# Optimization experiments

Measured on AMD Instinct MI355X. Metric: run time of the kernel, lower is better.

Reference implementation:

```python
import jax, jax.numpy as jnp
import numpy as np

B, N, C = 8, 4096, 1024
H = 16
D = C // H  # head_dim = 64
SCALE = D ** -0.5


def setup_inputs() -> dict:
    key = jax.random.key(0)
    ks = jax.random.split(key, 5)
    s = 0.02
    return {
        "x": jax.random.normal(ks[0], (B, N, C), dtype=jnp.float32),
        "Wq": jax.random.normal(ks[1], (C, C), dtype=jnp.float32) * s,
        "Wk": jax.random.normal(ks[2], (C, C), dtype=jnp.float32) * s,
        "Wv": jax.random.normal(ks[3], (C, C), dtype=jnp.float32) * s,
        "Wp": jax.random.normal(ks[4], (C, C), dtype=jnp.float32) * s,
        "bp": jnp.zeros((C,), dtype=jnp.float32),
    }


def reference(x, Wq, Wk, Wv, Wp, bp):
    b, n, c = x.shape
    # nn.Linear: y = x @ W^T (no bias for q/k/v)
    def split_heads(y):
        # (B,N,C) -> (B,N,H,D) -> permute(0,2,3,1) -> (B,H,D,N)
        return jnp.transpose(y.reshape(b, n, H, D), (0, 2, 3, 1))

    q = split_heads(x @ Wq.T)  # (B,H,D,N)
    k = split_heads(x @ Wk.T)  # (B,H,D,N)
    v = split_heads(x @ Wv.T)  # (B,H,D,N)

    # attn over head_dim (faithful to source layout): (B,H,D,D)
    attn = jnp.einsum('bhdn,bhen->bhde', q, k) * SCALE
    attn = jax.nn.softmax(attn, axis=-1)
    # (B,H,D,D) @ (B,H,D,N) -> (B,H,D,N); transpose(1,2) -> (B,D,H,N); reshape (B,N,C)
    out = jnp.einsum('bhde,bhen->bhdn', attn, v)
    out = jnp.transpose(out, (0, 2, 1, 3)).reshape(b, n, c)
    return out @ Wp.T + bp
```

## Files before the change

### kernel.cpp

```cpp
#include <hip/hip_runtime.h>


typedef __attribute__((ext_vector_type(4))) float f32x4;
typedef __attribute__((ext_vector_type(8))) _Float16 f16x8;
typedef __attribute__((ext_vector_type(4))) unsigned short u16x4;
typedef __attribute__((ext_vector_type(8))) unsigned short u16x8;

__device__ __forceinline__ unsigned short f2h(float f) {
  union { _Float16 h; unsigned short u; } v;
  v.h = (_Float16)f;
  return v.u;
}

__global__ void cvt_f32_f16(const float* __restrict__ in, unsigned short* __restrict__ out, int n) {
  int i = (blockIdx.x * blockDim.x + threadIdx.x) * 4;
  if (i >= n) return;
  float4 v = *(const float4*)(in + i);
  u16x4 o;
  o.x = f2h(v.x); o.y = f2h(v.y); o.z = f2h(v.z); o.w = f2h(v.w);
  *(u16x4*)(out + i) = o;
}

__global__ void cvt4_f32_f16(const float* __restrict__ s0, const float* __restrict__ s1,
                             const float* __restrict__ s2, const float* __restrict__ s3,
                             unsigned short* __restrict__ d0, unsigned short* __restrict__ d1,
                             unsigned short* __restrict__ d2, unsigned short* __restrict__ d3) {
  const float* src; unsigned short* dst;
  switch (blockIdx.y) {
    case 0: src = s0; dst = d0; break;
    case 1: src = s1; dst = d1; break;
    case 2: src = s2; dst = d2; break;
    default: src = s3; dst = d3; break;
  }
  int i = (blockIdx.x * blockDim.x + threadIdx.x) * 4;
  float4 v = *(const float4*)(src + i);
  u16x4 o;
  o.x = f2h(v.x); o.y = f2h(v.y); o.z = f2h(v.z); o.w = f2h(v.w);
  *(u16x4*)(dst + i) = o;
}

#define LDS_LD 68
enum { EPI_QKV = 0, EPI_F32_BIAS = 2 };

template <int EPI>
__global__ __launch_bounds__(256, 2) void gemm_bt(const unsigned short* __restrict__ A,
                                                  const unsigned short* __restrict__ Bt,
                                                  void* __restrict__ Cv,
                                                  const float* __restrict__ bias,
                                                  const int M, const int N, const int K) {
  __shared__ unsigned short lds[4 * 64 * LDS_LD];
  const int tid = threadIdx.x;
  const int wave = tid >> 6, lane = tid & 63;
  const int quad = lane >> 4, l15 = lane & 15;
  const int m0 = blockIdx.y * 128, n0 = blockIdx.x * 128;
  const int mb = (wave & 1) * 64, nb = (wave >> 1) * 64;

  const int sr = lane >> 2;
  const int sc = (lane & 3) ^ ((sr >> 1) & 3);

  const int swz = quad ^ ((l15 >> 1) & 3);
  int a_off[4], b_off[4];
#pragma unroll
  for (int t = 0; t < 4; t++) {
    a_off[t] = ((mb >> 4) + t) * 512 + (l15 * 4 + swz) * 8;
    b_off[t] = 4096 + ((nb >> 4) + t) * 512 + (l15 * 4 + swz) * 8;
  }

  const unsigned short* Ag = A + (size_t)(m0 + sr) * K + sc * 8;
  const unsigned short* Bg = Bt + (size_t)(n0 + sr) * K + sc * 8;

  f32x4 acc[4][4];
#pragma unroll
  for (int i = 0; i < 4; i++)
#pragma unroll
    for (int j = 0; j < 4; j++) acc[i][j] = f32x4{0.f, 0.f, 0.f, 0.f};

  for (int k0 = 0; k0 < K; k0 += 32) {
    __syncthreads();
#pragma unroll
    for (int rd = 0; rd < 2; rd++) {
      const int ch = rd * 4 + wave;
      __builtin_amdgcn_global_load_lds(
          (const __attribute__((address_space(1))) void*)(Ag + (size_t)ch * 16 * K + k0),
          (__attribute__((address_space(3))) void*)&lds[ch * 512], 16, 0, 0);
      __builtin_amdgcn_global_load_lds(
          (const __attribute__((address_space(1))) void*)(Bg + (size_t)ch * 16 * K + k0),
          (__attribute__((address_space(3))) void*)&lds[4096 + ch * 512], 16, 0, 0);
    }
    __syncthreads();

    f16x8 af[4], bf[4];
#pragma unroll
    for (int t = 0; t < 4; t++) {
      af[t] = *(const f16x8*)&lds[a_off[t]];
      bf[t] = *(const f16x8*)&lds[b_off[t]];
    }
#pragma unroll
    for (int mi = 0; mi < 4; mi++)
#pragma unroll
      for (int ni = 0; ni < 4; ni++)
        acc[mi][ni] = __builtin_amdgcn_mfma_f32_16x16x32_f16(af[mi], bf[ni], acc[mi][ni], 0, 0, 0);
  }

  __syncthreads();

  if (EPI == EPI_F32_BIAS) {
    float* C = (float*)Cv;
#pragma unroll
    for (int ni = 0; ni < 4; ni++) {
      const int col = n0 + nb + ni * 16 + l15;
      const float bv = bias[col];
#pragma unroll
      for (int mi = 0; mi < 4; mi++)
#pragma unroll
        for (int rr = 0; rr < 4; rr++) {
          const int row = m0 + mb + mi * 16 + quad * 4 + rr;
          C[(size_t)row * N + col] = acc[mi][ni][rr] + bv;
        }
    }
  } else {
    unsigned short* C = (unsigned short*)Cv;
    const bool isT = (n0 < 2048);
    unsigned short* w = &lds[wave * 64 * LDS_LD];
#pragma unroll
    for (int mi = 0; mi < 4; mi++)
#pragma unroll
      for (int ni = 0; ni < 4; ni++)
#pragma unroll
        for (int rr = 0; rr < 4; rr++) {
          const int rl = mi * 16 + quad * 4 + rr;
          const int cl = ni * 16 + l15;
          if (isT)
            w[cl * LDS_LD + rl] = f2h(acc[mi][ni][rr]);
          else
            w[rl * LDS_LD + cl] = f2h(acc[mi][ni][rr]);
        }
#pragma unroll
    for (int p = 0; p < 8; p++) {
      const int a = p * 8 + (lane >> 3);
      const int b8 = (lane & 7) * 8;
      u16x4 lo = *(const u16x4*)&w[a * LDS_LD + b8];
      u16x4 hi = *(const u16x4*)&w[a * LDS_LD + b8 + 4];
      size_t gi;
      if (isT)
        gi = (size_t)(n0 + nb + a) * M + (m0 + mb + b8);
      else
        gi = (size_t)2048 * 32768 + (size_t)(m0 + mb + a) * 1024 + (n0 - 2048 + nb + b8);
      *(u16x4*)&C[gi] = lo;
      *(u16x4*)&C[gi + 4] = hi;
    }
  }
}

__global__ __launch_bounds__(256) void attn_logits(const unsigned short* __restrict__ qkt,
                                                   float* __restrict__ pbuf) {
  const int h = blockIdx.x, b = blockIdx.y, s = blockIdx.z;
  const int tid = threadIdx.x;
  const int wave = tid >> 6, lane = tid & 63;
  const int quad = lane >> 4, l15 = lane & 15;

  f32x4 acc[4];
#pragma unroll
  for (int t = 0; t < 4; t++) acc[t] = f32x4{0.f, 0.f, 0.f, 0.f};

  const unsigned short* qp =
      qkt + (size_t)(h * 64 + wave * 16 + l15) * 32768 + b * 4096 + s * 256 + quad * 8;
  const unsigned short* kp[4];
#pragma unroll
  for (int et = 0; et < 4; et++)
    kp[et] = qkt + (size_t)(1024 + h * 64 + et * 16 + l15) * 32768 + b * 4096 + s * 256 + quad * 8;

#pragma unroll 2
  for (int k0 = 0; k0 < 256; k0 += 32) {
    f16x8 aq = *(const f16x8*)(qp + k0);
#pragma unroll
    for (int et = 0; et < 4; et++) {
      f16x8 bk = *(const f16x8*)(kp[et] + k0);
      acc[et] = __builtin_amdgcn_mfma_f32_16x16x32_f16(aq, bk, acc[et], 0, 0, 0);
    }
  }

  float* pb = pbuf + ((size_t)(b * 16 + h) * 16 + s) * 4096;
#pragma unroll
  for (int et = 0; et < 4; et++)
#pragma unroll
    for (int rr = 0; rr < 4; rr++)
      pb[(wave * 16 + quad * 4 + rr) * 64 + et * 16 + l15] = acc[et][rr];
}

__global__ __launch_bounds__(256) void attn_softmax(const float* __restrict__ pbuf,
                                                    unsigned short* __restrict__ pP) {
  const int bh = blockIdx.x >> 2, dg = blockIdx.x & 3;
  const int t = threadIdx.x;
  const int d = dg * 16 + (t >> 4), e4 = t & 15;
  const float* pb = pbuf + (size_t)bh * 65536 + d * 64 + e4 * 4;

  float v[4] = {0.f, 0.f, 0.f, 0.f};
  for (int s = 0; s < 16; s++) {
    float4 tt = *(const float4*)(pb + s * 4096);
    v[0] += tt.x; v[1] += tt.y; v[2] += tt.z; v[3] += tt.w;
  }
#pragma unroll
  for (int i = 0; i < 4; i++) v[i] *= 0.125f;

  float m = fmaxf(fmaxf(v[0], v[1]), fmaxf(v[2], v[3]));
#pragma unroll
  for (int o = 1; o < 16; o <<= 1) m = fmaxf(m, __shfl_xor(m, o, 16));
  float sum = 0.f;
#pragma unroll
  for (int i = 0; i < 4; i++) {
    v[i] = __expf(v[i] - m);
    sum += v[i];
  }
#pragma unroll
  for (int o = 1; o < 16; o <<= 1) sum += __shfl_xor(sum, o, 16);
  const float inv = 1.f / sum;

  u16x4 o4;
  o4.x = f2h(v[0] * inv); o4.y = f2h(v[1] * inv);
  o4.z = f2h(v[2] * inv); o4.w = f2h(v[3] * inv);
  *(u16x4*)(pP + (size_t)bh * 4096 + d * 64 + e4 * 4) = o4;
}

__global__ __launch_bounds__(256) void attn_pv(const unsigned short* __restrict__ pP,
                                               const unsigned short* __restrict__ vbuf,
                                               unsigned short* __restrict__ y) {
  __shared__ unsigned short tile[64 * 264];
  const int h = blockIdx.x, b = blockIdx.y, s = blockIdx.z;
  const int tid = threadIdx.x;
  const int wave = tid >> 6, lane = tid & 63;
  const int quad = lane >> 4, l15 = lane & 15;
  const int bh = b * 16 + h;

  const unsigned short* pp = pP + (size_t)bh * 4096 + (wave * 16 + l15) * 64 + quad * 8;
  f16x8 pa0 = *(const f16x8*)(pp);
  f16x8 pa1 = *(const f16x8*)(pp + 32);

  const unsigned short* vb =
      vbuf + (size_t)(b * 4096 + s * 256 + l15) * 1024 + h * 64 + quad * 8;

#pragma unroll 4
  for (int nt = 0; nt < 16; nt++) {
    const unsigned short* vp = vb + (size_t)nt * 16 * 1024;
    f16x8 v0 = *(const f16x8*)(vp);
    f16x8 v1 = *(const f16x8*)(vp + 32);
    f32x4 o = f32x4{0.f, 0.f, 0.f, 0.f};
    o = __builtin_amdgcn_mfma_f32_16x16x32_f16(pa0, v0, o, 0, 0, 0);
    o = __builtin_amdgcn_mfma_f32_16x16x32_f16(pa1, v1, o, 0, 0, 0);
    const int ncol = nt * 16 + l15;
#pragma unroll
    for (int rr = 0; rr < 4; rr++)
      tile[(wave * 16 + quad * 4 + rr) * 264 + ncol] = f2h(o[rr]);
  }
  __syncthreads();

  const int d = tid & 63, cc = tid >> 6;
  const int R = d * 64 + h * 4 + (s >> 2);
  unsigned short* dst =
      y + (size_t)b * 4194304 + (size_t)R * 1024 + (s & 3) * 256 + cc * 64;
  const unsigned short* srcp = &tile[d * 264 + cc * 64];
#pragma unroll
  for (int i = 0; i < 8; i++)
    *(u16x8*)(dst + i * 8) = *(const u16x8*)(srcp + i * 8);
}

extern "C" void kernel_launch(void* const* d_in, const int* in_sizes, int n_in, void* d_out,
                              int out_size, void* d_ws, size_t ws_size, hipStream_t stream) {
  (void)in_sizes; (void)n_in; (void)out_size; (void)ws_size;
  const float* x = (const float*)d_in[0];
  const float* Wq = (const float*)d_in[1];
  const float* Wk = (const float*)d_in[2];
  const float* Wv = (const float*)d_in[3];
  const float* Wp = (const float*)d_in[4];
  const float* bp = (const float*)d_in[5];

  char* ws = (char*)d_ws;
  unsigned short* xb = (unsigned short*)(ws);
  float* pbuf = (float*)(ws);
  unsigned short* yb = xb;
  unsigned short* qkt = (unsigned short*)(ws + (size_t)67108864);
  unsigned short* pP = qkt;
  unsigned short* vbuf = (unsigned short*)(ws + (size_t)201326592);
  unsigned short* wqkv = (unsigned short*)(ws + (size_t)268435456);
  unsigned short* wp = (unsigned short*)(ws + (size_t)274726912);

  cvt_f32_f16<<<32768, 256, 0, stream>>>(x, xb, 33554432);
  cvt4_f32_f16<<<dim3(1024, 4), 256, 0, stream>>>(Wq, Wk, Wv, Wp, wqkv, wqkv + 1048576,
                                                  wqkv + 2097152, wp);

  gemm_bt<EPI_QKV><<<dim3(24, 256), 256, 0, stream>>>(xb, wqkv, qkt, nullptr, 32768, 3072, 1024);

  attn_logits<<<dim3(16, 8, 16), 256, 0, stream>>>(qkt, pbuf);
  attn_softmax<<<512, 256, 0, stream>>>(pbuf, pP);
  attn_pv<<<dim3(16, 8, 16), 256, 0, stream>>>(pP, vbuf, yb);

  gemm_bt<EPI_F32_BIAS><<<dim3(8, 256), 256, 0, stream>>>(yb, wp, (float*)d_out, bp, 32768, 1024, 1024);
}
```

Measured before the change: 681.1 us.

## Replace GEMM with 256x256 double-buffered pipelined kernel and XCD-aware block mapping

Both projection GEMMs move to a 512-thread kernel with 256x256 tiles and a BK=64 double-buffered LDS pipeline. Global-to-LDS loads for the next tile are interleaved with MFMA phases using s_waitcnt, raw barriers and s_setprio. Block IDs are remapped so neighbouring tiles land on the same XCD, improving L2 reuse. The larger tile raises data reuse per load, but the 128-144KB of LDS limits occupancy and the hand-written wait counts are fragile.

```diff
diff --git a/kernel.cpp b/kernel.cpp
--- a/kernel.cpp
+++ b/kernel.cpp
@@ -39,115 +39,207 @@
   *(u16x4*)(dst + i) = o;
 }
 
-#define LDS_LD 68
 enum { EPI_QKV = 0, EPI_F32_BIAS = 2 };
 
+#define GLD(SRC, DST)                                                                   \
+  __builtin_amdgcn_global_load_lds((const __attribute__((address_space(1))) void*)(SRC), \
+                                   (__attribute__((address_space(3))) void*)(DST), 16, 0, 0)
+#define SBAR() asm volatile("s_barrier" ::: "memory")
+
 template <int EPI>
-__global__ __launch_bounds__(256, 2) void gemm_bt(const unsigned short* __restrict__ A,
+__global__ __launch_bounds__(512, 2) void gemm256(const unsigned short* __restrict__ A,
                                                   const unsigned short* __restrict__ Bt,
                                                   void* __restrict__ Cv,
                                                   const float* __restrict__ bias,
                                                   const int M, const int N, const int K) {
-  __shared__ unsigned short lds[4 * 64 * LDS_LD];
+  __shared__ unsigned short lds[EPI == EPI_QKV ? 73728 : 65536];
   const int tid = threadIdx.x;
-  const int wave = tid >> 6, lane = tid & 63;
+  const int w = tid >> 6, lane = tid & 63;
   const int quad = lane >> 4, l15 = lane & 15;
-  const int m0 = blockIdx.y * 128, n0 = blockIdx.x * 128;
-  const int mb = (wave & 1) * 64, nb = (wave >> 1) * 64;
-
-  const int sr = lane >> 2;
-  const int sc = (lane & 3) ^ ((sr >> 1) & 3);
-
-  const int swz = quad ^ ((l15 >> 1) & 3);
-  int a_off[4], b_off[4];
-#pragma unroll
-  for (int t = 0; t < 4; t++) {
-    a_off[t] = ((mb >> 4) + t) * 512 + (l15 * 4 + swz) * 8;
-    b_off[t] = 4096 + ((nb >> 4) + t) * 512 + (l15 * 4 + swz) * 8;
-  }
-
-  const unsigned short* Ag = A + (size_t)(m0 + sr) * K + sc * 8;
-  const unsigned short* Bg = Bt + (size_t)(n0 + sr) * K + sc * 8;
-
-  f32x4 acc[4][4];
-#pragma unroll
-  for (int i = 0; i < 4; i++)
-#pragma unroll
-    for (int j = 0; j < 4; j++) acc[i][j] = f32x4{0.f, 0.f, 0.f, 0.f};
-
-  for (int k0 = 0; k0 < K; k0 += 32) {
-    __syncthreads();
-#pragma unroll
-    for (int rd = 0; rd < 2; rd++) {
-      const int ch = rd * 4 + wave;
-      __builtin_amdgcn_global_load_lds(
-          (const __attribute__((address_space(1))) void*)(Ag + (size_t)ch * 16 * K + k0),
-          (__attribute__((address_space(3))) void*)&lds[ch * 512], 16, 0, 0);
-      __builtin_amdgcn_global_load_lds(
-          (const __attribute__((address_space(1))) void*)(Bg + (size_t)ch * 16 * K + k0),
-          (__attribute__((address_space(3))) void*)&lds[4096 + ch * 512], 16, 0, 0);
-    }
-    __syncthreads();
-
-    f16x8 af[4], bf[4];
-#pragma unroll
-    for (int t = 0; t < 4; t++) {
-      af[t] = *(const f16x8*)&lds[a_off[t]];
-      bf[t] = *(const f16x8*)&lds[b_off[t]];
-    }
-#pragma unroll
-    for (int mi = 0; mi < 4; mi++)
-#pragma unroll
-      for (int ni = 0; ni < 4; ni++)
-        acc[mi][ni] = __builtin_amdgcn_mfma_f32_16x16x32_f16(af[mi], bf[ni], acc[mi][ni], 0, 0, 0);
-  }
-
-  __syncthreads();
+  const int wm = w >> 2, wn = w & 3;
+
+  const int cpx = (int)gridDim.x >> 3;
+  const int wg = ((int)blockIdx.x & 7) * cpx + ((int)blockIdx.x >> 3);
+  const int mt = M >> 8;
+  const int bm = wg % mt, bn = wg / mt;
+  const int m0 = bm << 8, n0 = bn << 8;
+
+  const int srow = lane >> 3;
+  const unsigned short* aSrc = A + (size_t)(m0 + srow) * K + (((lane & 7) ^ srow) << 3);
+  const unsigned short* bSrc = Bt + (size_t)(n0 + srow) * K + (((lane & 7) ^ srow) << 3);
+
+  const int rbA = (w >> 2) * 128 + (w & 3) * 16;
+  const int rbB = (w >> 1) * 64 + (w & 1) * 16;
+
+  const int arow = (wm * 128 + l15) << 6;
+  const int brow = (wn * 64 + l15) << 6;
+  const int ak0 = (quad ^ (l15 & 7)) << 3;
+  const int ak1 = ((4 + quad) ^ (l15 & 7)) << 3;
+
+  f32x4 acc[8][4];
+#pragma unroll
+  for (int i = 0; i < 8; ++i)
+#pragma unroll
+    for (int j = 0; j < 4; ++j) acc[i][j] = f32x4{0.f, 0.f, 0.f, 0.f};
+  f16x8 af[4][2], bf[2][2][2];
+
+  const int NT = K >> 6;
+
+  GLD(aSrc + (size_t)rbA * K, &lds[rbA * 64]);
+  GLD(aSrc + (size_t)(rbA + 8) * K, &lds[(rbA + 8) * 64]);
+  GLD(bSrc + (size_t)rbB * K, &lds[16384 + rbB * 64]);
+  GLD(bSrc + (size_t)(rbB + 8) * K, &lds[16384 + (rbB + 8) * 64]);
+  GLD(bSrc + (size_t)(rbB + 32) * K, &lds[16384 + (rbB + 32) * 64]);
+  GLD(bSrc + (size_t)(rbB + 40) * K, &lds[16384 + (rbB + 40) * 64]);
+  GLD(aSrc + (size_t)(rbA + 64) * K, &lds[(rbA + 64) * 64]);
+  GLD(aSrc + (size_t)(rbA + 72) * K, &lds[(rbA + 72) * 64]);
+  asm volatile("s_waitcnt vmcnt(4)" ::: "memory");
+  SBAR();
+
+  for (int t = 0; t < NT; ++t) {
+    const int db = (t & 1) << 15;
+    const int sb = ((t + 1) & 1) << 15;
+    const int ks = (t + 1) << 6;
+    const bool st = (t + 1) < NT;
+    const bool last = (t + 1) == NT;
+
+#pragma unroll
+    for (int mi = 0; mi < 4; ++mi) {
+      af[mi][0] = *(const f16x8*)&lds[db + arow + mi * 1024 + ak0];
+      af[mi][1] = *(const f16x8*)&lds[db + arow + mi * 1024 + ak1];
+    }
+#pragma unroll
+    for (int nn = 0; nn < 2; ++nn) {
+      bf[0][nn][0] = *(const f16x8*)&lds[db + 16384 + brow + nn * 1024 + ak0];
+      bf[0][nn][1] = *(const f16x8*)&lds[db + 16384 + brow + nn * 1024 + ak1];
+    }
+    if (st) {
+      GLD(aSrc + (size_t)rbA * K + ks, &lds[sb + rbA * 64]);
+      GLD(aSrc + (size_t)(rbA + 8) * K + ks, &lds[sb + (rbA + 8) * 64]);
+    }
+    SBAR();
+    __builtin_amdgcn_s_setprio(1);
+#pragma unroll
+    for (int s = 0; s < 2; ++s)
+#pragma unroll
+      for (int mi = 0; mi < 4; ++mi)
+#pragma unroll
+        for (int nn = 0; nn < 2; ++nn)
+          acc[mi][nn] = __builtin_amdgcn_mfma_f32_16x16x32_f16(af[mi][s], bf[0][nn][s], acc[mi][nn], 0, 0, 0);
+    __builtin_amdgcn_s_setprio(0);
+    if (!last) asm volatile("s_waitcnt vmcnt(4)" ::: "memory");
+    else       asm volatile("s_waitcnt vmcnt(2)" ::: "memory");
+    SBAR();
+
+#pragma unroll
+    for (int nn = 0; nn < 2; ++nn) {
+      bf[1][nn][0] = *(const f16x8*)&lds[db + 16384 + brow + 2048 + nn * 1024 + ak0];
+      bf[1][nn][1] = *(const f16x8*)&lds[db + 16384 + brow + 2048 + nn * 1024 + ak1];
+    }
+    if (st) {
+      GLD(bSrc + (size_t)rbB * K + ks, &lds[sb + 16384 + rbB * 64]);
+      GLD(bSrc + (size_t)(rbB + 8) * K + ks, &lds[sb + 16384 + (rbB + 8) * 64]);
+    }
+    SBAR();
+    __builtin_amdgcn_s_setprio(1);
+#pragma unroll
+    for (int s = 0; s < 2; ++s)
+#pragma unroll
+      for (int mi = 0; mi < 4; ++mi)
+#pragma unroll
+        for (int nn = 0; nn < 2; ++nn)
+          acc[mi][2 + nn] = __builtin_amdgcn_mfma_f32_16x16x32_f16(af[mi][s], bf[1][nn][s], acc[mi][2 + nn], 0, 0, 0);
+    __builtin_amdgcn_s_setprio(0);
+    if (!last) asm volatile("s_waitcnt vmcnt(4)" ::: "memory");
+    else       asm volatile("s_waitcnt vmcnt(0)" ::: "memory");
+    SBAR();
+
+#pragma unroll
+    for (int mi = 0; mi < 4; ++mi) {
+      af[mi][0] = *(const f16x8*)&lds[db + arow + 4096 + mi * 1024 + ak0];
+      af[mi][1] = *(const f16x8*)&lds[db + arow + 4096 + mi * 1024 + ak1];
+    }
+    if (st) {
+      GLD(bSrc + (size_t)(rbB + 32) * K + ks, &lds[sb + 16384 + (rbB + 32) * 64]);
+      GLD(bSrc + (size_t)(rbB + 40) * K + ks, &lds[sb + 16384 + (rbB + 40) * 64]);
+    }
+    SBAR();
+    __builtin_amdgcn_s_setprio(1);
+#pragma unroll
+    for (int s = 0; s < 2; ++s)
+#pragma unroll
+      for (int mi = 0; mi < 4; ++mi)
+#pragma unroll
+        for (int nn = 0; nn < 2; ++nn)
+          acc[4 + mi][nn] = __builtin_amdgcn_mfma_f32_16x16x32_f16(af[mi][s], bf[0][nn][s], acc[4 + mi][nn], 0, 0, 0);
+    __builtin_amdgcn_s_setprio(0);
+    SBAR();
+
+    if (st) {
+      GLD(aSrc + (size_t)(rbA + 64) * K + ks, &lds[sb + (rbA + 64) * 64]);
+      GLD(aSrc + (size_t)(rbA + 72) * K + ks, &lds[sb + (rbA + 72) * 64]);
+    }
+    SBAR();
+    __builtin_amdgcn_s_setprio(1);
+#pragma unroll
+    for (int s = 0; s < 2; ++s)
+#pragma unroll
+      for (int mi = 0; mi < 4; ++mi)
+#pragma unroll
+        for (int nn = 0; nn < 2; ++nn)
+          acc[4 + mi][2 + nn] = __builtin_amdgcn_mfma_f32_16x16x32_f16(af[mi][s], bf[1][nn][s], acc[4 + mi][2 + nn], 0, 0, 0);
+    __builtin_amdgcn_s_setprio(0);
+    if (st) asm volatile("s_waitcnt vmcnt(4)" ::: "memory");
+    SBAR();
+  }
 
   if (EPI == EPI_F32_BIAS) {
     float* C = (float*)Cv;
 #pragma unroll
-    for (int ni = 0; ni < 4; ni++) {
-      const int col = n0 + nb + ni * 16 + l15;
+    for (int ni = 0; ni < 4; ++ni) {
+      const int col = n0 + wn * 64 + ni * 16 + l15;
       const float bv = bias[col];
 #pragma unroll
-      for (int mi = 0; mi < 4; mi++)
-#pragma unroll
-        for (int rr = 0; rr < 4; rr++) {
-          const int row = m0 + mb + mi * 16 + quad * 4 + rr;
+      for (int mi = 0; mi < 8; ++mi)
+#pragma unroll
+        for (int rr = 0; rr < 4; ++rr) {
+          const int row = m0 + wm * 128 + mi * 16 + quad * 4 + rr;
           C[(size_t)row * N + col] = acc[mi][ni][rr] + bv;
         }
     }
   } else {
     unsigned short* C = (unsigned short*)Cv;
     const bool isT = (n0 < 2048);
-    unsigned short* w = &lds[wave * 64 * LDS_LD];
-#pragma unroll
-    for (int mi = 0; mi < 4; mi++)
-#pragma unroll
-      for (int ni = 0; ni < 4; ni++)
-#pragma unroll
-        for (int rr = 0; rr < 4; rr++) {
-          const int rl = mi * 16 + quad * 4 + rr;
-          const int cl = ni * 16 + l15;
-          if (isT)
-            w[cl * LDS_LD + rl] = f2h(acc[mi][ni][rr]);
-          else
-            w[rl * LDS_LD + cl] = f2h(acc[mi][ni][rr]);
-        }
-#pragma unroll
-    for (int p = 0; p < 8; p++) {
-      const int a = p * 8 + (lane >> 3);
-      const int b8 = (lane & 7) * 8;
-      u16x4 lo = *(const u16x4*)&w[a * LDS_LD + b8];
-      u16x4 hi = *(const u16x4*)&w[a * LDS_LD + b8 + 4];
-      size_t gi;
-      if (isT)
-        gi = (size_t)(n0 + nb + a) * M + (m0 + mb + b8);
-      else
-        gi = (size_t)2048 * 32768 + (size_t)(m0 + mb + a) * 1024 + (n0 - 2048 + nb + b8);
-      *(u16x4*)&C[gi] = lo;
-      *(u16x4*)&C[gi + 4] = hi;
+    unsigned short* wreg = &lds[w * 9216];
+    if (isT) {
+#pragma unroll
+      for (int mi = 0; mi < 8; ++mi)
+#pragma unroll
+        for (int ni = 0; ni < 4; ++ni)
+#pragma unroll
+          for (int rr = 0; rr < 4; ++rr)
+            wreg[(ni * 16 + l15) * 136 + mi * 16 + quad * 4 + rr] = f2h(acc[mi][ni][rr]);
+#pragma unroll
+      for (int p = 0; p < 16; ++p) {
+        const int ch = p * 4 + quad;
+        u16x8 v = *(const u16x8*)&wreg[ch * 136 + l15 * 8];
+        *(u16x8*)&C[(size_t)(n0 + wn * 64 + ch) * M + m0 + wm * 128 + l15 * 8] = v;
+      }
+    } else {
+#pragma unroll
+      for (int mi = 0; mi < 8; ++mi)
+#pragma unroll
+        for (int ni = 0; ni < 4; ++ni)
+#pragma unroll
+          for (int rr = 0; rr < 4; ++rr)
+            wreg[(mi * 16 + quad * 4 + rr) * 72 + ni * 16 + l15] = f2h(acc[mi][ni][rr]);
+#pragma unroll
+      for (int p = 0; p < 16; ++p) {
+        const int tok = p * 8 + (lane >> 3);
+        u16x8 v = *(const u16x8*)&wreg[tok * 72 + (lane & 7) * 8];
+        *(u16x8*)&C[(size_t)2048 * M + (size_t)(m0 + wm * 128 + tok) * 1024 +
+                    (n0 - 2048) + wn * 64 + (lane & 7) * 8] = v;
+      }
     }
   }
 }
@@ -288,11 +380,11 @@
   cvt4_f32_f16<<<dim3(1024, 4), 256, 0, stream>>>(Wq, Wk, Wv, Wp, wqkv, wqkv + 1048576,
                                                   wqkv + 2097152, wp);
 
-  gemm_bt<EPI_QKV><<<dim3(24, 256), 256, 0, stream>>>(xb, wqkv, qkt, nullptr, 32768, 3072, 1024);
+  gemm256<EPI_QKV><<<1536, 512, 0, stream>>>(xb, wqkv, qkt, nullptr, 32768, 3072, 1024);
 
   attn_logits<<<dim3(16, 8, 16), 256, 0, stream>>>(qkt, pbuf);
   attn_softmax<<<512, 256, 0, stream>>>(pbuf, pP);
   attn_pv<<<dim3(16, 8, 16), 256, 0, stream>>>(pP, vbuf, yb);
 
-  gemm_bt<EPI_F32_BIAS><<<dim3(8, 256), 256, 0, stream>>>(yb, wp, (float*)d_out, bp, 32768, 1024, 1024);
-}
+  gemm256<EPI_F32_BIAS><<<512, 512, 0, stream>>>(yb, wp, (float*)d_out, bp, 32768, 1024, 1024);
+}
```

After: 634.4 us. 1.07x faster.
